# Optimization experiments

Hardware: AMD Instinct MI355X
Metric: run time of the kernel (lower is better)

The kernel has to match this reference:

```python
import jax, jax.numpy as jnp
import numpy as np

B, S, D = 2, 2048, 2048
H, DH = 16, 128          # n_heads, head_dim
HFF = 8192               # hidden_dim (SwiGLU)
EPS = 1e-5               # layer_norm_eps passed to AdvancedRMSNorm


def setup_inputs() -> dict:
    key = jax.random.key(0)
    ks = jax.random.split(key, 16)
    sd = lambda fan_in: 1.0 / np.sqrt(fan_in)
    inp = {
        "x": jax.random.normal(ks[0], (B, S, D), jnp.float32),
        # attention (torch Linear weights: [out, in])
        "q_w": jax.random.normal(ks[1], (D, D), jnp.float32) * sd(D),
        "k_w": jax.random.normal(ks[2], (D, D), jnp.float32) * sd(D),
        "v_w": jax.random.normal(ks[3], (D, D), jnp.float32) * sd(D),
        "o_w": jax.random.normal(ks[4], (D, D), jnp.float32) * sd(D),
        "temp": jnp.ones((H, 1, 1), jnp.float32),  # learnable per-head temperature
        # RMSNorm scales
        "ln1_w": jnp.ones((D,), jnp.float32),
        "ln2_w": jnp.ones((D,), jnp.float32),
        # SwiGLU
        "gate_w": jax.random.normal(ks[5], (HFF, D), jnp.float32) * sd(D),
        "up_w": jax.random.normal(ks[6], (HFF, D), jnp.float32) * sd(D),
        "gate2_w": jax.random.normal(ks[7], (HFF, D), jnp.float32) * sd(D),
        "down_w": jax.random.normal(ks[8], (D, HFF), jnp.float32) * sd(HFF),
        # gated residual connections (Linear with bias)
        "ag_w": jax.random.normal(ks[9], (D, D), jnp.float32) * sd(D),
        "ag_b": jnp.zeros((D,), jnp.float32),
        "fg_w": jax.random.normal(ks[10], (D, D), jnp.float32) * sd(D),
        "fg_b": jnp.zeros((D,), jnp.float32),
    }
    return inp


def _rmsnorm(x, w):
    rms = jnp.sqrt(jnp.mean(x * x, axis=-1, keepdims=True) + EPS)
    return w * (x / rms)


def _l2norm(x):
    # F.normalize(dim=-1): x / max(||x||_2, 1e-12)
    n = jnp.sqrt(jnp.sum(x * x, axis=-1, keepdims=True))
    return x / jnp.maximum(n, 1e-12)


def _block(x, q_w, k_w, v_w, o_w, temp, ln1_w, ln2_w,
           gate_w, up_w, gate2_w, down_w, ag_w, ag_b, fg_w, fg_b):
    # --- cosine-sim attention sublayer ---
    residual = x
    h = _rmsnorm(x, ln1_w)
    q = (h @ q_w.T).reshape(B, S, H, DH).transpose(0, 2, 1, 3)  # [B,H,S,DH]
    k = (h @ k_w.T).reshape(B, S, H, DH).transpose(0, 2, 1, 3)
    v = (h @ v_w.T).reshape(B, S, H, DH).transpose(0, 2, 1, 3)
    q = _l2norm(q)
    k = _l2norm(k)
    scores = jnp.einsum("bhqd,bhkd->bhqk", q, k) * temp  # temp [H,1,1] broadcasts
    causal = jnp.triu(jnp.ones((S, S), bool), k=1)
    scores = jnp.where(causal, -jnp.inf, scores)
    attn = jax.nn.softmax(scores, axis=-1)
    out = jnp.einsum("bhqk,bhkd->bhqd", attn, v)
    out = out.transpose(0, 2, 1, 3).reshape(B, S, D)
    attn_out = out @ o_w.T
    # gated residual: sigmoid(W a + b)*a + (1-g)*residual
    g = jax.nn.sigmoid(attn_out @ ag_w.T + ag_b)
    x = g * attn_out + (1.0 - g) * residual
    # --- SwiGLU sublayer ---
    residual = x
    h = _rmsnorm(x, ln2_w)
    gate = jax.nn.silu(h @ gate_w.T)
    up = h @ up_w.T
    gate2 = jax.nn.sigmoid(h @ gate2_w.T)
    ffn_out = (gate * up * gate2) @ down_w.T
    g = jax.nn.sigmoid(ffn_out @ fg_w.T + fg_b)
    return g * ffn_out + (1.0 - g) * residual


def reference(x, q_w, k_w, v_w, o_w, temp, ln1_w, ln2_w,
              gate_w, up_w, gate2_w, down_w, ag_w, ag_b, fg_w, fg_b):
    return _block(x, q_w, k_w, v_w, o_w, temp, ln1_w, ln2_w,
                  gate_w, up_w, gate2_w, down_w, ag_w, ag_b, fg_w, fg_b)
```

## Files before the change

### kernel.cpp

```cpp
#include <hip/hip_runtime.h>

typedef unsigned short u16;
typedef unsigned int u32;
using bf16x8 = __attribute__((ext_vector_type(8))) short;
using f32x4  = __attribute__((ext_vector_type(4))) float;

#define EPS 1e-5f

__device__ __forceinline__ u16 f2bf(float f) {
    union { float f; u32 u; } v; v.f = f;
    u32 r = v.u + 0x7FFFu + ((v.u >> 16) & 1u);
    return (u16)(r >> 16);
}
__device__ __forceinline__ float bf2f(u16 u) {
    union { u32 u; float f; } v; v.u = ((u32)u) << 16;
    return v.f;
}
__device__ __forceinline__ void gl16(const void* g, void* s) {
    __builtin_amdgcn_global_load_lds(
        (const __attribute__((address_space(1))) u32*)g,
        (__attribute__((address_space(3))) u32*)s, 16, 0, 0);
}
__device__ __forceinline__ float sigm(float x) { return 1.f / (1.f + __expf(-x)); }

__global__ void conv_bf16(const float* __restrict__ src, u16* __restrict__ dst, int n4) {
    int i = blockIdx.x * 256 + threadIdx.x;
    if (i >= n4) return;
    float4 v = reinterpret_cast<const float4*>(src)[i];
    u32 lo = (u32)f2bf(v.x) | ((u32)f2bf(v.y) << 16);
    u32 hi = (u32)f2bf(v.z) | ((u32)f2bf(v.w) << 16);
    reinterpret_cast<uint2*>(dst)[i] = make_uint2(lo, hi);
}

__global__ void conv3_bf16(const float* __restrict__ s0, const float* __restrict__ s1,
                           const float* __restrict__ s2, u16* __restrict__ d0,
                           u16* __restrict__ d1, u16* __restrict__ d2, int n4) {
    int i = blockIdx.x * 256 + threadIdx.x;
    if (i >= n4) return;
    const float* src = (blockIdx.y == 0) ? s0 : (blockIdx.y == 1) ? s1 : s2;
    u16* dst = (blockIdx.y == 0) ? d0 : (blockIdx.y == 1) ? d1 : d2;
    float4 v = reinterpret_cast<const float4*>(src)[i];
    u32 lo = (u32)f2bf(v.x) | ((u32)f2bf(v.y) << 16);
    u32 hi = (u32)f2bf(v.z) | ((u32)f2bf(v.w) << 16);
    reinterpret_cast<uint2*>(dst)[i] = make_uint2(lo, hi);
}

__global__ void rmsnorm_k(const float* __restrict__ x, const float* __restrict__ wt,
                          u16* __restrict__ out) {
    __shared__ float red[4];
    const int row = blockIdx.x, t = threadIdx.x;
    const float* xr = x + (size_t)row * 2048;
    float4 v0 = *reinterpret_cast<const float4*>(&xr[t * 8]);
    float4 v1 = *reinterpret_cast<const float4*>(&xr[t * 8 + 4]);
    float ss = v0.x*v0.x + v0.y*v0.y + v0.z*v0.z + v0.w*v0.w
             + v1.x*v1.x + v1.y*v1.y + v1.z*v1.z + v1.w*v1.w;
#pragma unroll
    for (int d = 1; d < 64; d <<= 1) ss += __shfl_xor(ss, d);
    if ((t & 63) == 0) red[t >> 6] = ss;
    __syncthreads();
    const float tot = red[0] + red[1] + red[2] + red[3];
    const float s = 1.f / sqrtf(tot * (1.f / 2048.f) + EPS);
    float4 w0 = *reinterpret_cast<const float4*>(&wt[t * 8]);
    float4 w1 = *reinterpret_cast<const float4*>(&wt[t * 8 + 4]);
    u32 o[4];
    o[0] = (u32)f2bf(v0.x * s * w0.x) | ((u32)f2bf(v0.y * s * w0.y) << 16);
    o[1] = (u32)f2bf(v0.z * s * w0.z) | ((u32)f2bf(v0.w * s * w0.w) << 16);
    o[2] = (u32)f2bf(v1.x * s * w1.x) | ((u32)f2bf(v1.y * s * w1.y) << 16);
    o[3] = (u32)f2bf(v1.z * s * w1.z) | ((u32)f2bf(v1.w * s * w1.w) << 16);
    *reinterpret_cast<uint4*>(&out[(size_t)row * 2048 + t * 8]) =
        make_uint4(o[0], o[1], o[2], o[3]);
}

__global__ void qk_l2norm(u16* __restrict__ qkv, const float* __restrict__ temp) {
    const int wid = blockIdx.x * 4 + (threadIdx.x >> 6);
    const int l = threadIdx.x & 63;
    const int n = wid >> 5;
    const int rem = wid & 31;
    const int which = rem >> 4;
    const int h = rem & 15;
    u16* p = qkv + (size_t)n * 6144 + which * 2048 + h * 128 + l * 2;
    u32 v = *reinterpret_cast<const u32*>(p);
    float f0 = bf2f((u16)(v & 0xffff)), f1 = bf2f((u16)(v >> 16));
    float ss = f0 * f0 + f1 * f1;
#pragma unroll
    for (int d = 1; d < 64; d <<= 1) ss += __shfl_xor(ss, d);
    float sc = 1.f / fmaxf(sqrtf(ss), 1e-12f);
    if (which == 0) sc *= temp[h];
    *reinterpret_cast<u32*>(p) = (u32)f2bf(f0 * sc) | ((u32)f2bf(f1 * sc) << 16);
}

__global__ __launch_bounds__(512, 1)
void gemm_big8(const u16* __restrict__ A, const u16* __restrict__ B,
               u16* __restrict__ outB, int M, int N, int K, int ldc) {
    extern __shared__ u16 lds[];
    const int nbn = N >> 8;
    const int nwg = (M >> 8) * nbn;
    const int orig = blockIdx.x;
    const int q8 = nwg >> 3, r8 = nwg & 7;
    const int xcd = orig & 7, lin = orig >> 3;
    const int wgid = (xcd < r8 ? xcd * (q8 + 1) : r8 * (q8 + 1) + (xcd - r8) * q8) + lin;
    const int g = wgid / (nbn << 2);
    const int rem = wgid - g * (nbn << 2);
    const int bn = rem >> 2;
    const int bm = (g << 2) + (rem & 3);

    const int t = threadIdx.x;
    const int w = t >> 6, l = t & 63;
    const int wr = w >> 2, wc = w & 3;
    const int lr = l & 15, lg = l >> 4;
    const int NT = K >> 6;

    const int srow = t >> 3;
    const int scg  = (t & 7) ^ (srow & 7);
    const u16* aS0 = A + (size_t)(bm * 256 + srow) * K + scg * 8;
    const u16* aS1 = aS0 + (size_t)128 * K;
    const u16* bS0 = B + (size_t)(bn * 256 + srow) * K + scg * 8;
    const u16* bS1 = bS0 + (size_t)128 * K;
    const size_t r64 = (size_t)64 * K;

#define STG(slot, src, ko) do {                                     \
        gl16((src) + (ko), (slot) + t * 8);                         \
        gl16((src) + (ko) + r64, (slot) + 4096 + t * 8);            \
    } while (0)
#define STG_TILE(bi, ko) do {                                       \
        u16* bb = lds + (bi) * 32768;                               \
        STG(bb + 16384, bS0, ko);                                   \
        STG(bb + 24576, bS1, ko);                                   \
        STG(bb + 0,     aS0, ko);                                   \
        STG(bb + 8192,  aS1, ko);                                   \
    } while (0)

    f32x4 acc[8][4];
#pragma unroll
    for (int i = 0; i < 8; i++)
#pragma unroll
        for (int j = 0; j < 4; j++) acc[i][j] = (f32x4){0.f, 0.f, 0.f, 0.f};

    const int xr = (lr & 7) << 4;
    const int kof[2] = { ((lg) << 4) ^ xr, ((4 + lg) << 4) ^ xr };

    STG_TILE(0, 0);
    asm volatile("s_waitcnt vmcnt(2)" ::: "memory");
    __builtin_amdgcn_s_barrier();

    for (int T = 0; T < NT; ++T) {
        const char* base = (const char*)lds + (size_t)(T & 1) * 65536;
        const int sbi = (T + 1) & 1;
        const bool st = (T + 1) < NT;
        const size_t ko = (size_t)(T + 1) * 64;
        const char* aB = base + wr * 16384;
        const char* bB = base + 32768 + (wc >> 1) * 16384 + (wc & 1) * 8192;
        bf16x8 bfr[4][2];

#pragma unroll
        for (int p = 0; p < 4; ++p) {
            const int ks = p >> 1, mh = p & 1;
            bf16x8 af[4];
#pragma unroll
            for (int m2 = 0; m2 < 4; m2++) {
                const int ra = mh * 64 + m2 * 16 + lr;
                af[m2] = *reinterpret_cast<const bf16x8*>(aB + ra * 128 + kof[ks]);
            }
            if (p == 0) {
#pragma unroll
                for (int n = 0; n < 4; n++) {
                    const int rb = n * 16 + lr;
                    bfr[n][0] = *reinterpret_cast<const bf16x8*>(bB + rb * 128 + kof[0]);
                    bfr[n][1] = *reinterpret_cast<const bf16x8*>(bB + rb * 128 + kof[1]);
                }
                if (st) STG_TILE(sbi, ko);
            }
            __builtin_amdgcn_s_barrier();
            __builtin_amdgcn_s_setprio(1);
#pragma unroll
            for (int m2 = 0; m2 < 4; m2++)
#pragma unroll
                for (int n = 0; n < 4; n++)
                    acc[mh * 4 + m2][n] = __builtin_amdgcn_mfma_f32_16x16x32_bf16(
                        af[m2], bfr[n][ks], acc[mh * 4 + m2][n], 0, 0, 0);
            __builtin_amdgcn_s_setprio(0);
            if (p == 0) {
                if (st) asm volatile("s_waitcnt vmcnt(8)" ::: "memory");
                else    asm volatile("s_waitcnt vmcnt(0)" ::: "memory");
            }
            if (p == 3 && st)
                asm volatile("s_waitcnt vmcnt(2)" ::: "memory");
            __builtin_amdgcn_s_barrier();
        }
    }
#undef STG
#undef STG_TILE

#pragma unroll
    for (int m = 0; m < 8; m++) {
        const int row = bm * 256 + wr * 128 + m * 16 + lg * 4;
#pragma unroll
        for (int n = 0; n < 4; n++) {
            const int col = bn * 256 + wc * 64 + n * 16 + lr;
#pragma unroll
            for (int q = 0; q < 4; q++)
                outB[(size_t)(row + q) * ldc + col] = f2bf(acc[m][n][q]);
        }
    }
}

template <int EPI>
__global__ __launch_bounds__(512, 1)
void gemm_u(const u16* __restrict__ A, const u16* __restrict__ B,
            float* __restrict__ outF, u16* __restrict__ outB,
            const float* __restrict__ bias, const float* __restrict__ addend,
            const float* __restrict__ resid, float* __restrict__ outG,
            int M, int N, int K, int ldc) {
    extern __shared__ u16 lds[];
    const int nbn = N >> 8;
    const int nwg = (M >> 7) * nbn;
    const int orig = blockIdx.x;
    const int q8 = nwg >> 3, r8 = nwg & 7;
    const int xcd = orig & 7, lin = orig >> 3;
    const int wgid = (xcd < r8 ? xcd * (q8 + 1) : r8 * (q8 + 1) + (xcd - r8) * q8) + lin;
    const int g = wgid / (nbn << 3);
    const int rem = wgid - g * (nbn << 3);
    const int bn = rem >> 3;
    const int bm = (g << 3) + (rem & 7);

    const int t = threadIdx.x;
    const int w = t >> 6, l = t & 63;
    const int wr = w >> 2, wc = w & 3;
    const int lr = l & 15, lg = l >> 4;
    const int NT = K >> 6;

    const int pr = t >> 3, ps = t & 7;
    const int sg = ps ^ (pr & 7);
    const u16* aSrc = A + (size_t)(bm * 128 + pr) * K + sg * 8;
    const u16* bSrc = B + (size_t)(bn * 256 + pr) * K + sg * 8;
    const size_t rowStep = (size_t)64 * K;

#define STG_A(bi, ko) do { u16* da = lds + (bi) * 24576 + t * 8;                 \
        gl16(aSrc + (ko), da); gl16(aSrc + rowStep + (ko), da + 4096); } while (0)
#define STG_B01(bi, ko) do { u16* db = lds + (bi) * 24576 + 8192 + t * 8;        \
        gl16(bSrc + (ko), db); gl16(bSrc + rowStep + (ko), db + 4096); } while (0)
#define STG_B23(bi, ko) do { u16* db = lds + (bi) * 24576 + 8192 + t * 8;        \
        gl16(bSrc + 2 * rowStep + (ko), db + 8192);                              \
        gl16(bSrc + 3 * rowStep + (ko), db + 12288); } while (0)

    f32x4 acc[4][4];
#pragma unroll
    for (int i = 0; i < 4; i++)
#pragma unroll
        for (int j = 0; j < 4; j++) acc[i][j] = (f32x4){0.f, 0.f, 0.f, 0.f};

    const int xr = (lr & 7) << 4;
    const int kof[2] = { ((lg) << 4) ^ xr, ((4 + lg) << 4) ^ xr };

    STG_A(0, 0); STG_B01(0, 0); STG_B23(0, 0);
    asm volatile("s_waitcnt vmcnt(0)" ::: "memory");
    __builtin_amdgcn_s_barrier();

    for (int T = 0; T < NT; ++T) {
        const char* bufA = (const char*)lds + (size_t)(T & 1) * 49152;
        const char* bufB = bufA + 16384;
        const int sbi = (T + 1) & 1;
        const bool st = (T + 1) < NT;
        const size_t ko = (size_t)(T + 1) * 64;
        bf16x8 bf[4][2];
#pragma unroll
        for (int n = 0; n < 4; n++) {
            const int rb = wc * 64 + n * 16 + lr;
            bf[n][0] = *reinterpret_cast<const bf16x8*>(bufB + rb * 128 + kof[0]);
            bf[n][1] = *reinterpret_cast<const bf16x8*>(bufB + rb * 128 + kof[1]);
        }
#pragma unroll
        for (int p = 0; p < 4; ++p) {
            const int ks = p >> 1, mh = p & 1;
            bf16x8 af[2];
#pragma unroll
            for (int m2 = 0; m2 < 2; m2++) {
                const int ra = wr * 64 + (mh * 2 + m2) * 16 + lr;
                af[m2] = *reinterpret_cast<const bf16x8*>(bufA + ra * 128 + kof[ks]);
            }
            if (st) {
                if (p == 0) STG_A(sbi, ko);
                if (p == 1) STG_B01(sbi, ko);
                if (p == 2) STG_B23(sbi, ko);
            }
            __builtin_amdgcn_s_setprio(1);
#pragma unroll
            for (int m2 = 0; m2 < 2; m2++)
#pragma unroll
                for (int n = 0; n < 4; n++)
                    acc[mh * 2 + m2][n] = __builtin_amdgcn_mfma_f32_16x16x32_bf16(
                        af[m2], bf[n][ks], acc[mh * 2 + m2][n], 0, 0, 0);
            __builtin_amdgcn_s_setprio(0);
        }
        if (st) {
            asm volatile("s_waitcnt vmcnt(0)" ::: "memory");
            __builtin_amdgcn_s_barrier();
        }
    }
#undef STG_A
#undef STG_B01
#undef STG_B23

#pragma unroll
    for (int m = 0; m < 4; m++) {
        const int row = bm * 128 + wr * 64 + m * 16 + lg * 4;
#pragma unroll
        for (int n = 0; n < 4; n++) {
            const int col = bn * 256 + wc * 64 + n * 16 + lr;
#pragma unroll
            for (int q = 0; q < 4; q++) {
                const size_t idx = (size_t)(row + q) * ldc + col;
                const float v = acc[m][n][q];
                if (EPI == 0) {
                    outB[idx] = f2bf(v);
                } else if (EPI == 1) {
                    outF[idx] = v;
                    outB[idx] = f2bf(v);
                } else {
                    const float g2 = sigm(v + bias[col]);
                    outG[idx] = g2 * addend[idx] + (1.f - g2) * resid[idx];
                }
            }
        }
    }
}

#define VSWZ(dh) (((((dh) >> 3) ^ (dh)) & 7) << 4)
__global__ __launch_bounds__(512) void flash_attn(const u16* __restrict__ qkv,
                                                  u16* __restrict__ out) {
    __shared__ u16 klds[2][64 * 128];
    __shared__ u16 vlds[2][128 * 64];
    __shared__ u16 plds[8][16 * 64];
    const int t = threadIdx.x, w = t >> 6, l = t & 63;
    const int lr = l & 15, lg = l >> 4;
    const int b0 = blockIdx.x;
    const int xcd = b0 & 7, i0 = b0 >> 3;
    const int bh = ((i0 & 3) << 3) | xcd;
    const int p = i0 >> 2;
    const int b = bh >> 4, h = bh & 15;
    const size_t base = (size_t)b * 2048;
    const int sr0 = t >> 4;
    const int sc0 = (t & 15) << 3;

    uint4 kreg0, kreg1, vreg0, vreg1;

#define STAGE_LOAD(KT) do {                                                          \
        const size_t gg = (base + (size_t)(KT) * 64 + sr0) * 6144 + h * 128 + sc0;   \
        kreg0 = *reinterpret_cast<const uint4*>(&qkv[gg + 2048]);                    \
        vreg0 = *reinterpret_cast<const uint4*>(&qkv[gg + 4096]);                    \
        kreg1 = *reinterpret_cast<const uint4*>(&qkv[gg + 32 * 6144 + 2048]);        \
        vreg1 = *reinterpret_cast<const uint4*>(&qkv[gg + 32 * 6144 + 4096]);        \
    } while (0)

#define STAGE_WRITE(BUF) do {                                                                     \
        char* kb = (char*)&klds[BUF][0];                                                          \
        char* vb = (char*)&vlds[BUF][0];                                                          \
        *reinterpret_cast<uint4*>(kb + ((sr0 * 256 + sc0 * 2) ^ ((sr0 & 7) << 4))) = kreg0;       \
        *reinterpret_cast<uint4*>(kb + (((sr0 + 32) * 256 + sc0 * 2) ^ ((sr0 & 7) << 4))) = kreg1;\
        union { uint4 u; u16 s[8]; } vv;                                                          \
        vv.u = vreg0;                                                                             \
        _Pragma("unroll")                                                                         \
        for (int jj = 0; jj < 8; jj++) {                                                          \
            const int dh = sc0 + jj;                                                              \
            *reinterpret_cast<u16*>(vb + ((dh * 128 + sr0 * 2) ^ VSWZ(dh))) = vv.s[jj];           \
        }                                                                                         \
        vv.u = vreg1;                                                                             \
        _Pragma("unroll")                                                                         \
        for (int jj = 0; jj < 8; jj++) {                                                          \
            const int dh = sc0 + jj;                                                              \
            *reinterpret_cast<u16*>(vb + ((dh * 128 + (sr0 + 32) * 2) ^ VSWZ(dh))) = vv.s[jj];    \
        }                                                                                         \
    } while (0)

    for (int phase = 0; phase < 2; ++phase) {
        const int qt = phase ? (15 - p) : p;
        const int last = 2 * qt + 1;
        const int qrow = qt * 128 + w * 16 + lr;
        const int qr0 = qt * 128 + w * 16 + lg * 4;
        bf16x8 qf[4];
#pragma unroll
        for (int kk = 0; kk < 4; kk++)
            qf[kk] = *reinterpret_cast<const bf16x8*>(
                &qkv[(base + qrow) * 6144 + h * 128 + kk * 32 + lg * 8]);
        f32x4 o[8];
#pragma unroll
        for (int i = 0; i < 8; i++) o[i] = (f32x4){0.f, 0.f, 0.f, 0.f};
        float m[4] = {-1e30f, -1e30f, -1e30f, -1e30f};
        float ls[4] = {0.f, 0.f, 0.f, 0.f};

        STAGE_LOAD(0);
        int cur = 0;
        STAGE_WRITE(0);
        __syncthreads();

        for (int kt = 0; kt <= last; ++kt) {
            if (kt < last) STAGE_LOAD(kt + 1);
            const char* kb = (const char*)&klds[cur][0];
            const char* vb = (const char*)&vlds[cur][0];
            f32x4 s[4];
#pragma unroll
            for (int nf = 0; nf < 4; nf++) {
                f32x4 a = (f32x4){0.f, 0.f, 0.f, 0.f};
                const int kv = nf * 16 + lr;
#pragma unroll
                for (int kk = 0; kk < 4; kk++) {
                    bf16x8 kf = *reinterpret_cast<const bf16x8*>(
                        kb + ((kv * 256 + kk * 64 + lg * 16) ^ ((kv & 7) << 4)));
                    a = __builtin_amdgcn_mfma_f32_16x16x32_bf16(qf[kk], kf, a, 0, 0, 0);
                }
                s[nf] = a;
            }
            if (kt >= 2 * qt) {
#pragma unroll
                for (int nf = 0; nf < 4; nf++) {
                    const int kvi = kt * 64 + nf * 16 + lr;
#pragma unroll
                    for (int q = 0; q < 4; q++)
                        if (kvi > qr0 + q) s[nf][q] = -1e30f;
                }
            }
            float mx[4] = {-1e30f, -1e30f, -1e30f, -1e30f};
#pragma unroll
            for (int nf = 0; nf < 4; nf++)
#pragma unroll
                for (int q = 0; q < 4; q++) mx[q] = fmaxf(mx[q], s[nf][q]);
#pragma unroll
            for (int q = 0; q < 4; q++) {
#pragma unroll
                for (int d = 1; d < 16; d <<= 1) mx[q] = fmaxf(mx[q], __shfl_xor(mx[q], d));
            }
            float fac[4], rs[4];
#pragma unroll
            for (int q = 0; q < 4; q++) {
                const float mn = fmaxf(m[q], mx[q]);
                fac[q] = __expf(m[q] - mn);
                m[q] = mn;
                rs[q] = 0.f;
            }
#pragma unroll
            for (int nf = 0; nf < 4; nf++) {
#pragma unroll
                for (int q = 0; q < 4; q++) {
                    const float pv = __expf(s[nf][q] - m[q]);
                    s[nf][q] = pv;
                    rs[q] += pv;
                }
            }
#pragma unroll
            for (int nf = 0; nf < 4; nf++) {
                const int col = nf * 16 + lr;
#pragma unroll
                for (int q = 0; q < 4; q++) {
                    const int row = lg * 4 + q;
                    *reinterpret_cast<u16*>((char*)&plds[w][0] +
                        ((row * 128 + col * 2) ^ ((row & 7) << 4))) = f2bf(s[nf][q]);
                }
            }
#pragma unroll
            for (int q = 0; q < 4; q++) {
#pragma unroll
                for (int d = 1; d < 16; d <<= 1) rs[q] += __shfl_xor(rs[q], d);
                ls[q] = ls[q] * fac[q] + rs[q];
            }
#pragma unroll
            for (int nf2 = 0; nf2 < 8; nf2++)
#pragma unroll
                for (int q = 0; q < 4; q++) o[nf2][q] *= fac[q];
#pragma unroll
            for (int ks = 0; ks < 2; ks++) {
                bf16x8 pf = *reinterpret_cast<const bf16x8*>((char*)&plds[w][0] +
                    ((lr * 128 + ks * 64 + lg * 16) ^ ((lr & 7) << 4)));
#pragma unroll
                for (int nf2 = 0; nf2 < 8; nf2++) {
                    const int dh = nf2 * 16 + lr;
                    bf16x8 vf = *reinterpret_cast<const bf16x8*>(
                        vb + ((dh * 128 + ks * 64 + lg * 16) ^ VSWZ(dh)));
                    o[nf2] = __builtin_amdgcn_mfma_f32_16x16x32_bf16(pf, vf, o[nf2], 0, 0, 0);
                }
            }
            if (kt < last) STAGE_WRITE(cur ^ 1);
            __syncthreads();
            cur ^= 1;
        }
#pragma unroll
        for (int nf2 = 0; nf2 < 8; nf2++) {
            const int col = h * 128 + nf2 * 16 + lr;
#pragma unroll
            for (int q = 0; q < 4; q++) {
                const float v = o[nf2][q] / ls[q];
                out[(base + qr0 + q) * 2048 + col] = f2bf(v);
            }
        }
        __syncthreads();
    }
#undef STAGE_LOAD
#undef STAGE_WRITE
}

__global__ void swiglu_comb(const u16* __restrict__ f3, u16* __restrict__ comb) {
    const size_t u = (size_t)blockIdx.x * 256 + threadIdx.x;
    const size_t n = u >> 8;
    const int f = (int)(u & 255) << 3;
    const u16* gp = f3 + n * 6144 + f;
    union { uint4 q; u16 s[8]; } g, up, g2;
    g.q  = *reinterpret_cast<const uint4*>(gp);
    up.q = *reinterpret_cast<const uint4*>(gp + 2048);
    g2.q = *reinterpret_cast<const uint4*>(gp + 4096);
    u32 r[4];
#pragma unroll
    for (int i = 0; i < 4; i++) {
        float a0 = bf2f(g.s[2 * i]),     a1 = bf2f(g.s[2 * i + 1]);
        float b0 = bf2f(up.s[2 * i]),    b1 = bf2f(up.s[2 * i + 1]);
        float c0 = bf2f(g2.s[2 * i]),    c1 = bf2f(g2.s[2 * i + 1]);
        float r0 = a0 * sigm(a0) * b0 * sigm(c0);
        float r1 = a1 * sigm(a1) * b1 * sigm(c1);
        r[i] = (u32)f2bf(r0) | ((u32)f2bf(r1) << 16);
    }
    *reinterpret_cast<uint4*>(comb + n * 8192 + f) = make_uint4(r[0], r[1], r[2], r[3]);
}

extern "C" void kernel_launch(void* const* d_in, const int* in_sizes, int n_in,
                              void* d_out, int out_size, void* d_ws, size_t ws_size,
                              hipStream_t stream) {
    const float* x      = (const float*)d_in[0];
    const float* q_w    = (const float*)d_in[1];
    const float* k_w    = (const float*)d_in[2];
    const float* v_w    = (const float*)d_in[3];
    const float* o_w    = (const float*)d_in[4];
    const float* temp   = (const float*)d_in[5];
    const float* ln1_w  = (const float*)d_in[6];
    const float* ln2_w  = (const float*)d_in[7];
    const float* gate_w = (const float*)d_in[8];
    const float* up_w   = (const float*)d_in[9];
    const float* gate2_w= (const float*)d_in[10];
    const float* down_w = (const float*)d_in[11];
    const float* ag_w   = (const float*)d_in[12];
    const float* ag_b   = (const float*)d_in[13];
    const float* fg_w   = (const float*)d_in[14];
    const float* fg_b   = (const float*)d_in[15];

    const int GEMM_LDS = 98304;
    const int BIG_LDS  = 131072;
    (void)hipFuncSetAttribute(reinterpret_cast<const void*>(&gemm_u<0>),
                              hipFuncAttributeMaxDynamicSharedMemorySize, GEMM_LDS);
    (void)hipFuncSetAttribute(reinterpret_cast<const void*>(&gemm_u<1>),
                              hipFuncAttributeMaxDynamicSharedMemorySize, GEMM_LDS);
    (void)hipFuncSetAttribute(reinterpret_cast<const void*>(&gemm_u<2>),
                              hipFuncAttributeMaxDynamicSharedMemorySize, GEMM_LDS);
    (void)hipFuncSetAttribute(reinterpret_cast<const void*>(&gemm_big8),
                              hipFuncAttributeMaxDynamicSharedMemorySize, BIG_LDS);

    char* ws = (char*)d_ws;
    u16*  Wbuf = (u16*)(ws);
    u16*  hbuf = (u16*)(ws + 33554432);
    float* x1  = (float*)(ws + 50331648);
    u16*  combo= (u16*)(ws + 83886080);
    char* E    = ws + 150994944;
    char* F    = ws + 201326592;
    u16*  ffb  = (u16*)(ws + 234881024);

    u16*   qkvact = (u16*)E;
    float* aof    = (float*)E;
    u16*   aob    = (u16*)(E + 33554432);
    u16*   ffn3q  = (u16*)E;
    u16*   attnb  = (u16*)F;
    float* fff    = (float*)F;

    float* outp = (float*)d_out;
    const size_t DD = 2048ull * 2048ull;
    const int cg_d = (int)(DD / 4) / 256;
    const int GRID_BIG = 16 * 24;
    const int GRID_SM  = 32 * 8;

    hipLaunchKernelGGL(rmsnorm_k, dim3(4096), dim3(256), 0, stream, x, ln1_w, hbuf);

    hipLaunchKernelGGL(conv3_bf16, dim3(cg_d, 3), dim3(256), 0, stream,
                       q_w, k_w, v_w, Wbuf, Wbuf + DD, Wbuf + 2 * DD, (int)(DD / 4));
    hipLaunchKernelGGL(gemm_big8, dim3(GRID_BIG), dim3(512), BIG_LDS, stream,
                       hbuf, Wbuf, qkvact, 4096, 6144, 2048, 6144);

    hipLaunchKernelGGL(qk_l2norm, dim3(32768), dim3(256), 0, stream, qkvact, temp);

    hipLaunchKernelGGL(flash_attn, dim3(256), dim3(512), 0, stream, qkvact, attnb);

    hipLaunchKernelGGL(conv_bf16, dim3(cg_d), dim3(256), 0, stream, o_w, Wbuf, (int)(DD / 4));
    hipLaunchKernelGGL((gemm_u<1>), dim3(GRID_SM), dim3(512), GEMM_LDS, stream,
                       attnb, Wbuf, aof, aob,
                       (const float*)nullptr, (const float*)nullptr, (const float*)nullptr,
                       (float*)nullptr, 4096, 2048, 2048, 2048);

    hipLaunchKernelGGL(conv_bf16, dim3(cg_d), dim3(256), 0, stream, ag_w, Wbuf, (int)(DD / 4));
    hipLaunchKernelGGL((gemm_u<2>), dim3(GRID_SM), dim3(512), GEMM_LDS, stream,
                       aob, Wbuf, (float*)nullptr, (u16*)nullptr,
                       ag_b, aof, x, x1, 4096, 2048, 2048, 2048);

    hipLaunchKernelGGL(rmsnorm_k, dim3(4096), dim3(256), 0, stream, x1, ln2_w, hbuf);

    for (int qd = 0; qd < 4; qd++) {
        const size_t wofs = (size_t)qd * 2048 * 2048;
        hipLaunchKernelGGL(conv3_bf16, dim3(cg_d, 3), dim3(256), 0, stream,
                           gate_w + wofs, up_w + wofs, gate2_w + wofs,
                           Wbuf, Wbuf + 2048 * 2048, Wbuf + 2ull * 2048 * 2048, (int)(DD / 4));
        hipLaunchKernelGGL(gemm_big8, dim3(GRID_BIG), dim3(512), BIG_LDS, stream,
                           hbuf, Wbuf, ffn3q, 4096, 6144, 2048, 6144);
        hipLaunchKernelGGL(swiglu_comb, dim3(4096), dim3(256), 0, stream, ffn3q, combo + qd * 2048);
    }

    hipLaunchKernelGGL(conv_bf16, dim3(16384), dim3(256), 0, stream, down_w, Wbuf, (int)(2048ull * 8192 / 4));
    hipLaunchKernelGGL((gemm_u<1>), dim3(GRID_SM), dim3(512), GEMM_LDS, stream,
                       combo, Wbuf, fff, ffb,
                       (const float*)nullptr, (const float*)nullptr, (const float*)nullptr,
                       (float*)nullptr, 4096, 2048, 8192, 2048);

    hipLaunchKernelGGL(conv_bf16, dim3(cg_d), dim3(256), 0, stream, fg_w, Wbuf, (int)(DD / 4));
    hipLaunchKernelGGL((gemm_u<2>), dim3(GRID_SM), dim3(512), GEMM_LDS, stream,
                       ffb, Wbuf, (float*)nullptr, (u16*)nullptr,
                       fg_b, fff, x1, outp, 4096, 2048, 2048, 2048);
}
```

Before: 1.182 ms.

## Fuse SwiGLU elementwise into FFN GEMM over gate/up/gate2 panels

Replaces the big QKV/FFN GEMM with a fused kernel that computes the gate, up and gate2 panels one after another for each output tile. It keeps the silu(gate)*up partial packed in registers and writes the final combined SwiGLU product directly. This removes the intermediate 6144-wide activation buffer and the separate swiglu_comb pass, and halves the number of FFN launches by processing two weight quarters per launch. The QKV projection now uses the generic gemm_u<0> path instead. The costs are a simpler single-barrier pipeline with vmcnt(0) waits, extra register pressure, and bf16 rounding of the intermediate product.

```diff
diff --git a/kernel.cpp b/kernel.cpp
--- a/kernel.cpp
+++ b/kernel.cpp
@@ -15,6 +15,9 @@
 __device__ __forceinline__ float bf2f(u16 u) {
     union { u32 u; float f; } v; v.u = ((u32)u) << 16;
     return v.f;
+}
+__device__ __forceinline__ u32 pack2(float a, float b) {
+    return (u32)f2bf(a) | ((u32)f2bf(b) << 16);
 }
 __device__ __forceinline__ void gl16(const void* g, void* s) {
     __builtin_amdgcn_global_load_lds(
@@ -63,10 +66,10 @@
     float4 w0 = *reinterpret_cast<const float4*>(&wt[t * 8]);
     float4 w1 = *reinterpret_cast<const float4*>(&wt[t * 8 + 4]);
     u32 o[4];
-    o[0] = (u32)f2bf(v0.x * s * w0.x) | ((u32)f2bf(v0.y * s * w0.y) << 16);
-    o[1] = (u32)f2bf(v0.z * s * w0.z) | ((u32)f2bf(v0.w * s * w0.w) << 16);
-    o[2] = (u32)f2bf(v1.x * s * w1.x) | ((u32)f2bf(v1.y * s * w1.y) << 16);
-    o[3] = (u32)f2bf(v1.z * s * w1.z) | ((u32)f2bf(v1.w * s * w1.w) << 16);
+    o[0] = pack2(v0.x * s * w0.x, v0.y * s * w0.y);
+    o[1] = pack2(v0.z * s * w0.z, v0.w * s * w0.w);
+    o[2] = pack2(v1.x * s * w1.x, v1.y * s * w1.y);
+    o[3] = pack2(v1.z * s * w1.z, v1.w * s * w1.w);
     *reinterpret_cast<uint4*>(&out[(size_t)row * 2048 + t * 8]) =
         make_uint4(o[0], o[1], o[2], o[3]);
 }
@@ -86,23 +89,23 @@
     for (int d = 1; d < 64; d <<= 1) ss += __shfl_xor(ss, d);
     float sc = 1.f / fmaxf(sqrtf(ss), 1e-12f);
     if (which == 0) sc *= temp[h];
-    *reinterpret_cast<u32*>(p) = (u32)f2bf(f0 * sc) | ((u32)f2bf(f1 * sc) << 16);
+    *reinterpret_cast<u32*>(p) = pack2(f0 * sc, f1 * sc);
 }
 
 __global__ __launch_bounds__(512, 1)
-void gemm_big8(const u16* __restrict__ A, const u16* __restrict__ B,
-               u16* __restrict__ outB, int M, int N, int K, int ldc) {
+void gemm_swiglu(const u16* __restrict__ A, const u16* __restrict__ W0,
+                 const u16* __restrict__ W1, u16* __restrict__ combo, int K) {
     extern __shared__ u16 lds[];
-    const int nbn = N >> 8;
-    const int nwg = (M >> 8) * nbn;
     const int orig = blockIdx.x;
-    const int q8 = nwg >> 3, r8 = nwg & 7;
     const int xcd = orig & 7, lin = orig >> 3;
-    const int wgid = (xcd < r8 ? xcd * (q8 + 1) : r8 * (q8 + 1) + (xcd - r8) * q8) + lin;
-    const int g = wgid / (nbn << 2);
-    const int rem = wgid - g * (nbn << 2);
+    const int wgid = xcd * 32 + lin;
+    const int qsel = wgid & 1;
+    const int tix = wgid >> 1;
+    const int g = tix >> 5;
+    const int rem = tix & 31;
     const int bn = rem >> 2;
     const int bm = (g << 2) + (rem & 3);
+    const u16* B = qsel ? W1 : W0;
 
     const int t = threadIdx.x;
     const int w = t >> 6, l = t & 63;
@@ -114,92 +117,121 @@
     const int scg  = (t & 7) ^ (srow & 7);
     const u16* aS0 = A + (size_t)(bm * 256 + srow) * K + scg * 8;
     const u16* aS1 = aS0 + (size_t)128 * K;
-    const u16* bS0 = B + (size_t)(bn * 256 + srow) * K + scg * 8;
-    const u16* bS1 = bS0 + (size_t)128 * K;
     const size_t r64 = (size_t)64 * K;
 
 #define STG(slot, src, ko) do {                                     \
         gl16((src) + (ko), (slot) + t * 8);                         \
         gl16((src) + (ko) + r64, (slot) + 4096 + t * 8);            \
     } while (0)
-#define STG_TILE(bi, ko) do {                                       \
-        u16* bb = lds + (bi) * 32768;                               \
-        STG(bb + 16384, bS0, ko);                                   \
-        STG(bb + 24576, bS1, ko);                                   \
-        STG(bb + 0,     aS0, ko);                                   \
-        STG(bb + 8192,  aS1, ko);                                   \
-    } while (0)
-
-    f32x4 acc[8][4];
-#pragma unroll
-    for (int i = 0; i < 8; i++)
-#pragma unroll
-        for (int j = 0; j < 4; j++) acc[i][j] = (f32x4){0.f, 0.f, 0.f, 0.f};
 
     const int xr = (lr & 7) << 4;
     const int kof[2] = { ((lg) << 4) ^ xr, ((4 + lg) << 4) ^ xr };
 
-    STG_TILE(0, 0);
-    asm volatile("s_waitcnt vmcnt(2)" ::: "memory");
-    __builtin_amdgcn_s_barrier();
-
-    for (int T = 0; T < NT; ++T) {
-        const char* base = (const char*)lds + (size_t)(T & 1) * 65536;
-        const int sbi = (T + 1) & 1;
-        const bool st = (T + 1) < NT;
-        const size_t ko = (size_t)(T + 1) * 64;
-        const char* aB = base + wr * 16384;
-        const char* bB = base + 32768 + (wc >> 1) * 16384 + (wc & 1) * 8192;
-        bf16x8 bfr[4][2];
-
-#pragma unroll
-        for (int p = 0; p < 4; ++p) {
-            const int ks = p >> 1, mh = p & 1;
-            bf16x8 af[4];
-#pragma unroll
-            for (int m2 = 0; m2 < 4; m2++) {
-                const int ra = mh * 64 + m2 * 16 + lr;
-                af[m2] = *reinterpret_cast<const bf16x8*>(aB + ra * 128 + kof[ks]);
-            }
-            if (p == 0) {
-#pragma unroll
-                for (int n = 0; n < 4; n++) {
-                    const int rb = n * 16 + lr;
-                    bfr[n][0] = *reinterpret_cast<const bf16x8*>(bB + rb * 128 + kof[0]);
-                    bfr[n][1] = *reinterpret_cast<const bf16x8*>(bB + rb * 128 + kof[1]);
-                }
-                if (st) STG_TILE(sbi, ko);
-            }
-            __builtin_amdgcn_s_barrier();
-            __builtin_amdgcn_s_setprio(1);
-#pragma unroll
-            for (int m2 = 0; m2 < 4; m2++)
+    f32x4 acc[8][4];
+    u32 pk[8][4][2];
+
+    for (int pan = 0; pan < 3; ++pan) {
+        const u16* bS0 = B + (size_t)(pan * 2048 + bn * 256 + srow) * K + scg * 8;
+        const u16* bS1 = bS0 + (size_t)128 * K;
+        {
+            u16* bb = lds;
+            STG(bb + 16384, bS0, 0);
+            STG(bb + 24576, bS1, 0);
+            STG(bb + 0,     aS0, 0);
+            STG(bb + 8192,  aS1, 0);
+        }
+        if (pan == 1) {
+#pragma unroll
+            for (int m = 0; m < 8; m++)
 #pragma unroll
                 for (int n = 0; n < 4; n++)
-                    acc[mh * 4 + m2][n] = __builtin_amdgcn_mfma_f32_16x16x32_bf16(
-                        af[m2], bfr[n][ks], acc[mh * 4 + m2][n], 0, 0, 0);
-            __builtin_amdgcn_s_setprio(0);
-            if (p == 0) {
-                if (st) asm volatile("s_waitcnt vmcnt(8)" ::: "memory");
-                else    asm volatile("s_waitcnt vmcnt(0)" ::: "memory");
-            }
-            if (p == 3 && st)
-                asm volatile("s_waitcnt vmcnt(2)" ::: "memory");
-            __builtin_amdgcn_s_barrier();
+#pragma unroll
+                    for (int h = 0; h < 2; h++) {
+                        const float a0 = acc[m][n][2 * h], a1 = acc[m][n][2 * h + 1];
+                        pk[m][n][h] = pack2(a0 * sigm(a0), a1 * sigm(a1));
+                    }
+        } else if (pan == 2) {
+#pragma unroll
+            for (int m = 0; m < 8; m++)
+#pragma unroll
+                for (int n = 0; n < 4; n++)
+#pragma unroll
+                    for (int h = 0; h < 2; h++) {
+                        const u32 sv = pk[m][n][h];
+                        const float t0 = bf2f((u16)(sv & 0xffff)) * acc[m][n][2 * h];
+                        const float t1 = bf2f((u16)(sv >> 16)) * acc[m][n][2 * h + 1];
+                        pk[m][n][h] = pack2(t0, t1);
+                    }
+        }
+        asm volatile("s_waitcnt vmcnt(0)" ::: "memory");
+        __builtin_amdgcn_s_barrier();
+
+#pragma unroll
+        for (int i = 0; i < 8; i++)
+#pragma unroll
+            for (int j = 0; j < 4; j++) acc[i][j] = (f32x4){0.f, 0.f, 0.f, 0.f};
+
+        for (int T = 0; T < NT; ++T) {
+            const char* base = (const char*)lds + (size_t)(T & 1) * 65536;
+            u16* sb = lds + ((T + 1) & 1) * 32768;
+            const bool st = (T + 1) < NT;
+            const size_t ko = (size_t)(T + 1) * 64;
+            const char* aB = base + wr * 16384;
+            const char* bB = base + 32768 + (wc >> 1) * 16384 + (wc & 1) * 8192;
+            bf16x8 bfr[4][2];
+#pragma unroll
+            for (int n = 0; n < 4; n++) {
+                const int rb = n * 16 + lr;
+                bfr[n][0] = *reinterpret_cast<const bf16x8*>(bB + rb * 128 + kof[0]);
+                bfr[n][1] = *reinterpret_cast<const bf16x8*>(bB + rb * 128 + kof[1]);
+            }
+#pragma unroll
+            for (int p = 0; p < 4; ++p) {
+                const int ks = p >> 1, mh = p & 1;
+                bf16x8 af[4];
+#pragma unroll
+                for (int m2 = 0; m2 < 4; m2++) {
+                    const int ra = mh * 64 + m2 * 16 + lr;
+                    af[m2] = *reinterpret_cast<const bf16x8*>(aB + ra * 128 + kof[ks]);
+                }
+                if (st) {
+                    if (p == 0) STG(sb + 16384, bS0, ko);
+                    if (p == 1) STG(sb + 24576, bS1, ko);
+                    if (p == 2) STG(sb + 0,     aS0, ko);
+                    if (p == 3) STG(sb + 8192,  aS1, ko);
+                }
+                __builtin_amdgcn_s_setprio(1);
+#pragma unroll
+                for (int m2 = 0; m2 < 4; m2++)
+#pragma unroll
+                    for (int n = 0; n < 4; n++)
+                        acc[mh * 4 + m2][n] = __builtin_amdgcn_mfma_f32_16x16x32_bf16(
+                            af[m2], bfr[n][ks], acc[mh * 4 + m2][n], 0, 0, 0);
+                __builtin_amdgcn_s_setprio(0);
+            }
+            if (st) {
+                asm volatile("s_waitcnt vmcnt(0)" ::: "memory");
+                __builtin_amdgcn_s_barrier();
+            }
         }
     }
 #undef STG
-#undef STG_TILE
-
+
+    const int cbase = qsel * 2048 + bn * 256;
 #pragma unroll
     for (int m = 0; m < 8; m++) {
         const int row = bm * 256 + wr * 128 + m * 16 + lg * 4;
 #pragma unroll
         for (int n = 0; n < 4; n++) {
-            const int col = bn * 256 + wc * 64 + n * 16 + lr;
-#pragma unroll
-            for (int q = 0; q < 4; q++)
-                outB[(size_t)(row + q) * ldc + col] = f2bf(acc[m][n][q]);
+            const int col = cbase + wc * 64 + n * 16 + lr;
+#pragma unroll
+            for (int h = 0; h < 2; h++) {
+                const u32 tv = pk[m][n][h];
+                const float o0 = bf2f((u16)(tv & 0xffff)) * sigm(acc[m][n][2 * h]);
+                const float o1 = bf2f((u16)(tv >> 16)) * sigm(acc[m][n][2 * h + 1]);
+                combo[(size_t)(row + 2 * h) * 8192 + col] = f2bf(o0);
+                combo[(size_t)(row + 2 * h + 1) * 8192 + col] = f2bf(o1);
+            }
         }
     }
 }
@@ -497,28 +529,6 @@
 #undef STAGE_WRITE
 }
 
-__global__ void swiglu_comb(const u16* __restrict__ f3, u16* __restrict__ comb) {
-    const size_t u = (size_t)blockIdx.x * 256 + threadIdx.x;
-    const size_t n = u >> 8;
-    const int f = (int)(u & 255) << 3;
-    const u16* gp = f3 + n * 6144 + f;
-    union { uint4 q; u16 s[8]; } g, up, g2;
-    g.q  = *reinterpret_cast<const uint4*>(gp);
-    up.q = *reinterpret_cast<const uint4*>(gp + 2048);
-    g2.q = *reinterpret_cast<const uint4*>(gp + 4096);
-    u32 r[4];
-#pragma unroll
-    for (int i = 0; i < 4; i++) {
-        float a0 = bf2f(g.s[2 * i]),     a1 = bf2f(g.s[2 * i + 1]);
-        float b0 = bf2f(up.s[2 * i]),    b1 = bf2f(up.s[2 * i + 1]);
-        float c0 = bf2f(g2.s[2 * i]),    c1 = bf2f(g2.s[2 * i + 1]);
-        float r0 = a0 * sigm(a0) * b0 * sigm(c0);
-        float r1 = a1 * sigm(a1) * b1 * sigm(c1);
-        r[i] = (u32)f2bf(r0) | ((u32)f2bf(r1) << 16);
-    }
-    *reinterpret_cast<uint4*>(comb + n * 8192 + f) = make_uint4(r[0], r[1], r[2], r[3]);
-}
-
 extern "C" void kernel_launch(void* const* d_in, const int* in_sizes, int n_in,
                               void* d_out, int out_size, void* d_ws, size_t ws_size,
                               hipStream_t stream) {
@@ -540,15 +550,15 @@
     const float* fg_b   = (const float*)d_in[15];
 
     const int GEMM_LDS = 98304;
-    const int BIG_LDS  = 131072;
+    const int SW_LDS   = 131072;
     (void)hipFuncSetAttribute(reinterpret_cast<const void*>(&gemm_u<0>),
                               hipFuncAttributeMaxDynamicSharedMemorySize, GEMM_LDS);
     (void)hipFuncSetAttribute(reinterpret_cast<const void*>(&gemm_u<1>),
                               hipFuncAttributeMaxDynamicSharedMemorySize, GEMM_LDS);
     (void)hipFuncSetAttribute(reinterpret_cast<const void*>(&gemm_u<2>),
                               hipFuncAttributeMaxDynamicSharedMemorySize, GEMM_LDS);
-    (void)hipFuncSetAttribute(reinterpret_cast<const void*>(&gemm_big8),
-                              hipFuncAttributeMaxDynamicSharedMemorySize, BIG_LDS);
+    (void)hipFuncSetAttribute(reinterpret_cast<const void*>(&gemm_swiglu),
+                              hipFuncAttributeMaxDynamicSharedMemorySize, SW_LDS);
 
     char* ws = (char*)d_ws;
     u16*  Wbuf = (u16*)(ws);
@@ -562,22 +572,24 @@
     u16*   qkvact = (u16*)E;
     float* aof    = (float*)E;
     u16*   aob    = (u16*)(E + 33554432);
-    u16*   ffn3q  = (u16*)E;
+    u16*   Wffn2  = (u16*)E;
     u16*   attnb  = (u16*)F;
     float* fff    = (float*)F;
 
     float* outp = (float*)d_out;
     const size_t DD = 2048ull * 2048ull;
     const int cg_d = (int)(DD / 4) / 256;
-    const int GRID_BIG = 16 * 24;
+    const int GRID_BIG = 32 * 24;
     const int GRID_SM  = 32 * 8;
 
     hipLaunchKernelGGL(rmsnorm_k, dim3(4096), dim3(256), 0, stream, x, ln1_w, hbuf);
 
     hipLaunchKernelGGL(conv3_bf16, dim3(cg_d, 3), dim3(256), 0, stream,
                        q_w, k_w, v_w, Wbuf, Wbuf + DD, Wbuf + 2 * DD, (int)(DD / 4));
-    hipLaunchKernelGGL(gemm_big8, dim3(GRID_BIG), dim3(512), BIG_LDS, stream,
-                       hbuf, Wbuf, qkvact, 4096, 6144, 2048, 6144);
+    hipLaunchKernelGGL((gemm_u<0>), dim3(GRID_BIG), dim3(512), GEMM_LDS, stream,
+                       hbuf, Wbuf, (float*)nullptr, qkvact,
+                       (const float*)nullptr, (const float*)nullptr, (const float*)nullptr,
+                       (float*)nullptr, 4096, 6144, 2048, 6144);
 
     hipLaunchKernelGGL(qk_l2norm, dim3(32768), dim3(256), 0, stream, qkvact, temp);
 
@@ -596,14 +608,17 @@
 
     hipLaunchKernelGGL(rmsnorm_k, dim3(4096), dim3(256), 0, stream, x1, ln2_w, hbuf);
 
-    for (int qd = 0; qd < 4; qd++) {
-        const size_t wofs = (size_t)qd * 2048 * 2048;
+    for (int d = 0; d < 2; d++) {
+        const size_t w0 = (size_t)(2 * d) * 2048 * 2048;
+        const size_t w1 = (size_t)(2 * d + 1) * 2048 * 2048;
         hipLaunchKernelGGL(conv3_bf16, dim3(cg_d, 3), dim3(256), 0, stream,
-                           gate_w + wofs, up_w + wofs, gate2_w + wofs,
+                           gate_w + w0, up_w + w0, gate2_w + w0,
                            Wbuf, Wbuf + 2048 * 2048, Wbuf + 2ull * 2048 * 2048, (int)(DD / 4));
-        hipLaunchKernelGGL(gemm_big8, dim3(GRID_BIG), dim3(512), BIG_LDS, stream,
-                           hbuf, Wbuf, ffn3q, 4096, 6144, 2048, 6144);
-        hipLaunchKernelGGL(swiglu_comb, dim3(4096), dim3(256), 0, stream, ffn3q, combo + qd * 2048);
+        hipLaunchKernelGGL(conv3_bf16, dim3(cg_d, 3), dim3(256), 0, stream,
+                           gate_w + w1, up_w + w1, gate2_w + w1,
+                           Wffn2, Wffn2 + 2048 * 2048, Wffn2 + 2ull * 2048 * 2048, (int)(DD / 4));
+        hipLaunchKernelGGL(gemm_swiglu, dim3(256), dim3(512), SW_LDS, stream,
+                           hbuf, Wbuf, Wffn2, combo + (size_t)d * 2 * 2048, 2048);
     }
 
     hipLaunchKernelGGL(conv_bf16, dim3(16384), dim3(256), 0, stream, down_w, Wbuf, (int)(2048ull * 8192 / 4));
```

New measurement: 1.045 ms. -11.6%, faster.
